# Kernel optimization log

Hardware: AMD Instinct MI355X
Metric: run time of the kernel (lower is better)

Reference implementation:

```python
import jax, jax.numpy as jnp
import numpy as np

N = 131072       # total nodes (B graphs x P nodes)
P = 4096         # nodes per graph
B = 32           # graphs in batch
E = 2097152      # edges (avg degree 16)
IN_DIM = 64
HID = 128
OUT = 16
EPS = 1e-5
SLOPE = 0.01


def _degrees(idx):
    # structural degree, clamped to min 1 (as DGL GraphConv does)
    d = jax.ops.segment_sum(jnp.ones((E,), jnp.float32), idx, num_segments=N)
    return jnp.maximum(d, 1.0)


def _graph_conv(x, W, src, dst, ew):
    # DGL GraphConv, norm='both', bias=False, with scalar edge weights:
    # h = D_out^{-1/2} x ; m_v = sum_{(u->v)} w_e h_u ; out = (D_in^{-1/2} m) W
    h = x * jax.lax.rsqrt(_degrees(src))[:, None]
    m = jax.ops.segment_sum(ew[:, None] * h[src], dst, num_segments=N)  # [N, F]
    return (m * jax.lax.rsqrt(_degrees(dst))[:, None]) @ W


def _graph_norm(x, gamma, beta, alpha):
    # GraphNorm (Cai et al. / PyG, batch=None): stats over all nodes per feature
    mu = jnp.mean(x, axis=0)
    c = x - alpha * mu
    var = jnp.mean(c * c, axis=0)
    return c * jax.lax.rsqrt(var + EPS) * gamma + beta


def _mean_nodes(h, gid):
    # per-graph mean readout; every graph has exactly P nodes
    return jax.ops.segment_sum(h, gid, num_segments=B) / P


def setup_inputs() -> dict:
    key = jax.random.key(0)
    ks = jax.random.split(key, 8)
    src = jax.random.randint(ks[0], (E,), 0, N, dtype=jnp.int32)
    # keep edges within each 4096-node graph block (batched DGL graph)
    dst = (src // P) * P + jax.random.randint(ks[1], (E,), 0, P, dtype=jnp.int32)
    features = jax.random.normal(ks[2], (N, IN_DIM), jnp.float32)
    edge_weights = jax.random.uniform(ks[3], (E,), jnp.float32)
    # kaiming/xavier-scale init approximations
    W1 = jax.random.normal(ks[4], (IN_DIM, HID), jnp.float32) * np.sqrt(2.0 / IN_DIM)
    W2 = jax.random.normal(ks[5], (HID, HID), jnp.float32) * np.sqrt(2.0 / HID)
    Wc = jax.random.normal(ks[6], (OUT, 2 * HID), jnp.float32) * np.sqrt(1.0 / (2 * HID))
    ones = jnp.ones((HID,), jnp.float32)
    zeros = jnp.zeros((HID,), jnp.float32)
    return {
        'features': features, 'edge_weights': edge_weights, 'src': src, 'dst': dst,
        'W1': W1, 'W2': W2, 'Wc': Wc,
        'gamma1': ones, 'beta1': zeros, 'alpha1': ones,
        'gamma2': ones, 'beta2': zeros, 'alpha2': ones,
    }


def reference(features, edge_weights, src, dst, W1, W2, Wc,
              gamma1, beta1, alpha1, gamma2, beta2, alpha2):
    gid = jnp.arange(N, dtype=jnp.int32) // P  # node -> graph id
    h1 = _graph_conv(features, W1, src, dst, edge_weights)
    h1 = jax.nn.leaky_relu(_graph_norm(h1, gamma1, beta1, alpha1), SLOPE)
    r1 = _mean_nodes(h1, gid)                  # [B, HID]
    h2 = _graph_conv(h1, W2, src, dst, edge_weights)
    h2 = jax.nn.leaky_relu(_graph_norm(h2, gamma2, beta2, alpha2), SLOPE)
    r2 = _mean_nodes(h2, gid)                  # [B, HID]
    readouts = jnp.concatenate([r1, r2], axis=1)  # [B, 2*HID]
    return readouts @ Wc.T                     # [B, OUT]
```

## Files before the change

### kernel.cpp

```cpp
#include <hip/hip_runtime.h>
#include <hip/hip_fp16.h>

constexpr int NN   = 131072;
constexpr int PP   = 4096;
constexpr int BG   = 32;
constexpr int EE   = 2097152;
constexpr int IND  = 64;
constexpr int HH   = 128;
constexpr int CAP  = 81920;
constexpr float EPSV   = 1e-5f;
constexpr float SLOPEV = 0.01f;

typedef _Float16 h16x8 __attribute__((ext_vector_type(8)));
typedef float f32x4  __attribute__((ext_vector_type(4)));

__device__ __forceinline__ __half2 bits2h(unsigned u) { __half2 h; *(unsigned*)&h = u; return h; }
__device__ __forceinline__ unsigned h2bits(__half2 h) { return *(unsigned*)&h; }

template <int K>
__device__ __forceinline__ void packw_body(const float* __restrict__ W,
                                           unsigned short* __restrict__ pw, int t) {
    if (t >= K * 16) return;
    int lane = t & 63, nt = (t >> 6) & 7, kt = t >> 9;
    int kbase = kt * 32 + ((lane >> 4) & 3) * 8;
    int col   = nt * 16 + (lane & 15);
    for (int j = 0; j < 8; j++)
        pw[t * 8 + j] = __half_as_ushort(__float2half_rn(W[(kbase + j) * HH + col]));
}

__global__ __launch_bounds__(256) void k_prep(const float* __restrict__ features,
                                              unsigned* __restrict__ f16x,
                                              const float* __restrict__ W1,
                                              unsigned short* __restrict__ pw1,
                                              const float* __restrict__ W2,
                                              unsigned short* __restrict__ pw2,
                                              int* __restrict__ gcur,
                                              float* __restrict__ racc,
                                              unsigned* __restrict__ csr2) {
    int b = blockIdx.x, t = threadIdx.x;
    if (b < 8192) {
        int i = b * 256 + t;
        float4 v = ((const float4*)features)[i];
        __half2 lo = __floats2half2_rn(v.x, v.y);
        __half2 hi = __floats2half2_rn(v.z, v.w);
        ((uint2*)f16x)[i] = make_uint2(h2bits(lo), h2bits(hi));
        return;
    }
    if (b == 8192) {
        if (t < BG) gcur[t * 16] = t * CAP;
        for (int i = t; i < 2 * BG * HH; i += 256) racc[i] = 0.f;
        return;
    }
    if (b < 8197) { packw_body<64>(W1, pw1, (b - 8193) * 256 + t); return; }
    if (b < 8205) { packw_body<128>(W2, pw2, (b - 8197) * 256 + t); return; }
    ((uint4*)csr2)[(b - 8205) * 256 + t] = make_uint4(0, 0, 0, 0);
}

__global__ __launch_bounds__(256) void k_part(const int* __restrict__ src,
                                              const int* __restrict__ dst,
                                              const float* __restrict__ ew,
                                              int* __restrict__ gcur,
                                              uint2* __restrict__ recs) {
    __shared__ int cnt[32];
    __shared__ int start[32];
    __shared__ int gbase[32];
    __shared__ uint2 stage[4096];
    int t = threadIdx.x;
    int ebase = blockIdx.x * 4096;
    if (t < 32) cnt[t] = 0;
    __syncthreads();
    int es[16]; int ed[16]; float ev[16];
#pragma unroll
    for (int k = 0; k < 16; k++) {
        int e = ebase + k * 256 + t;
        es[k] = src[e]; ed[k] = dst[e]; ev[k] = ew[e];
        atomicAdd(&cnt[es[k] >> 12], 1);
    }
    __syncthreads();
    if (t == 0) {
        int run = 0;
        for (int g = 0; g < 32; g++) { start[g] = run; run += cnt[g]; }
    }
    __syncthreads();
    if (t < 32) {
        gbase[t] = atomicAdd(&gcur[t * 16], cnt[t]);
        cnt[t] = start[t];
    }
    __syncthreads();
#pragma unroll
    for (int k = 0; k < 16; k++) {
        int g = es[k] >> 12;
        int pos = atomicAdd(&cnt[g], 1);
        stage[pos] = make_uint2((unsigned)(es[k] & 4095) | ((unsigned)(ed[k] & 4095) << 12) |
                                ((unsigned)g << 24), __float_as_uint(ev[k]));
    }
    __syncthreads();
    for (int i = t; i < 4096; i += 256) {
        uint2 r = stage[i];
        int g = r.x >> 24;
        recs[gbase[g] + (i - start[g])] = r;
    }
}

__global__ __launch_bounds__(1024) void k_hist(const uint2* __restrict__ recs,
                                               const int* __restrict__ gcur,
                                               int* __restrict__ shist,
                                               int* __restrict__ dhist) {
    __shared__ int hs[4096];
    __shared__ int hd[4096];
    int t = threadIdx.x;
    int g = blockIdx.x >> 3, c = blockIdx.x & 7;
    int n = gcur[g * 16] - g * CAP;
    int lo = (n * c) >> 3, hi = (n * (c + 1)) >> 3;
    ((int4*)hs)[t] = make_int4(0, 0, 0, 0);
    ((int4*)hd)[t] = make_int4(0, 0, 0, 0);
    __syncthreads();
    const uint2* base = recs + (size_t)g * CAP;
    for (int i = lo + t; i < hi; i += 1024) {
        unsigned x = base[i].x;
        atomicAdd(&hs[x & 4095], 1);
        atomicAdd(&hd[(x >> 12) & 4095], 1);
    }
    __syncthreads();
    ((int4*)(shist + (size_t)blockIdx.x * 4096))[t] = ((int4*)hs)[t];
    ((int4*)(dhist + (size_t)blockIdx.x * 4096))[t] = ((int4*)hd)[t];
}

__global__ __launch_bounds__(1024) void k_offs(int* __restrict__ shist,
                                               int* __restrict__ dhist,
                                               float* __restrict__ rs_s,
                                               float* __restrict__ rsd,
                                               int* __restrict__ degd,
                                               int* __restrict__ offs) {
    __shared__ int partial[1024];
    int t = threadIdx.x, g = blockIdx.x;
    int sdeg[4] = {0, 0, 0, 0}, ddeg[4] = {0, 0, 0, 0};
#pragma unroll
    for (int c = 0; c < 8; c++) {
        int4 sv = ((const int4*)(shist + (size_t)(g * 8 + c) * 4096))[t];
        int4 dv = ((const int4*)(dhist + (size_t)(g * 8 + c) * 4096))[t];
        sdeg[0] += sv.x; sdeg[1] += sv.y; sdeg[2] += sv.z; sdeg[3] += sv.w;
        ddeg[0] += dv.x; ddeg[1] += dv.y; ddeg[2] += dv.z; ddeg[3] += dv.w;
    }
    int pdeg[4];
#pragma unroll
    for (int j = 0; j < 4; j++) {
        int idx = t * 4 + j;
        int vs = sdeg[j]; if (vs < 1) vs = 1;
        rs_s[g * PP + idx] = rsqrtf((float)vs);
        int vd = ddeg[j]; if (vd < 1) vd = 1;
        rsd[g * PP + idx]  = rsqrtf((float)vd);
        pdeg[j] = (ddeg[j] + 3) & ~3;
        degd[g * PP + idx] = pdeg[j];
    }
    partial[t] = pdeg[0] + pdeg[1] + pdeg[2] + pdeg[3];
    __syncthreads();
    for (int off = 1; off < 1024; off <<= 1) {
        int v = partial[t];
        int add = (t >= off) ? partial[t - off] : 0;
        __syncthreads();
        partial[t] = v + add;
        __syncthreads();
    }
    int run = (t == 0) ? 0 : partial[t - 1];
#pragma unroll
    for (int j = 0; j < 4; j++) {
        int idx = t * 4 + j;
        offs[g * PP + idx] = g * CAP + run;
        int nb = run;
        for (int c = 0; c < 8; c++) {
            size_t hidx = (size_t)(g * 8 + c) * 4096 + idx;
            int v = dhist[hidx];
            dhist[hidx] = nb;
            nb += v;
        }
        run += pdeg[j];
    }
}

__global__ __launch_bounds__(1024) void k_place(const uint2* __restrict__ recs,
                                                const int* __restrict__ gcur,
                                                const int* __restrict__ dhist,
                                                const float* __restrict__ rs_s,
                                                unsigned* __restrict__ csr2) {
    __shared__ int cur[4096];
    __shared__ float rss[4096];
    int t = threadIdx.x;
    int g = blockIdx.x >> 3, c = blockIdx.x & 7;
    int n = gcur[g * 16] - g * CAP;
    int lo = (n * c) >> 3, hi = (n * (c + 1)) >> 3;
    ((int4*)cur)[t] = ((const int4*)(dhist + (size_t)blockIdx.x * 4096))[t];
    ((float4*)rss)[t] = ((const float4*)(rs_s + (size_t)g * PP))[t];
    __syncthreads();
    const uint2* base = recs + (size_t)g * CAP;
    unsigned* cbase = csr2 + (size_t)g * CAP;
    for (int i = lo + t; i < hi; i += 1024) {
        uint2 r = base[i];
        int sl = r.x & 4095, dl = (r.x >> 12) & 4095;
        int pos = atomicAdd(&cur[dl], 1);
        float wf = __uint_as_float(r.y) * rss[sl];
        cbase[pos] = (unsigned)sl | ((unsigned)__half_as_ushort(__float2half(wf)) << 16);
    }
}

__device__ __forceinline__ void edge_acc(unsigned rec, uint2 q, __half2& P01, __half2& P23) {
    unsigned wb = __builtin_amdgcn_perm(rec, rec, 0x03020302u);
    __half2 w2 = bits2h(wb);
    P01 = __hfma2(w2, bits2h(q.x), P01);
    P23 = __hfma2(w2, bits2h(q.y), P23);
}

template <int ROWW>
__device__ __forceinline__ void agg_dual(const uint2* __restrict__ gb, unsigned loff,
                                         const uint4* __restrict__ cs4,
                                         int oa, int ca, int ob, int cb,
                                         __half2& A01, __half2& A23,
                                         __half2& B01, __half2& B23) {
    A01 = __float2half2_rn(0.f); A23 = A01; B01 = A01; B23 = A01;
    unsigned a4 = ((unsigned)oa) >> 2, b4 = ((unsigned)ob) >> 2;
    int c0 = ca < cb ? ca : cb;
    int cm = ca < cb ? cb : ca;
    int nq = c0 >> 2;
    uint4 ra = cs4[a4], rb = cs4[b4];
    for (int k = 0; k < nq; k++) {
        uint2 qa0 = gb[(ra.x & 4095u) * ROWW + loff];
        uint2 qa1 = gb[(ra.y & 4095u) * ROWW + loff];
        uint2 qa2 = gb[(ra.z & 4095u) * ROWW + loff];
        uint2 qa3 = gb[(ra.w & 4095u) * ROWW + loff];
        uint2 qb0 = gb[(rb.x & 4095u) * ROWW + loff];
        uint2 qb1 = gb[(rb.y & 4095u) * ROWW + loff];
        uint2 qb2 = gb[(rb.z & 4095u) * ROWW + loff];
        uint2 qb3 = gb[(rb.w & 4095u) * ROWW + loff];
        uint4 na = cs4[a4 + k + 1];
        uint4 nb = cs4[b4 + k + 1];
        edge_acc(ra.x, qa0, A01, A23); edge_acc(ra.y, qa1, A01, A23);
        edge_acc(ra.z, qa2, A01, A23); edge_acc(ra.w, qa3, A01, A23);
        edge_acc(rb.x, qb0, B01, B23); edge_acc(rb.y, qb1, B01, B23);
        edge_acc(rb.z, qb2, B01, B23); edge_acc(rb.w, qb3, B01, B23);
        ra = na; rb = nb;
    }
    if (cm > c0) {
        bool an = ca > cb;
        unsigned t4 = an ? a4 : b4;
        int kq1 = cm >> 2;
        __half2 E01 = __float2half2_rn(0.f), E23 = E01;
        uint4 rr = cs4[t4 + nq];
        for (int k = nq; k < kq1; k++) {
            uint2 q0 = gb[(rr.x & 4095u) * ROWW + loff];
            uint2 q1 = gb[(rr.y & 4095u) * ROWW + loff];
            uint2 q2 = gb[(rr.z & 4095u) * ROWW + loff];
            uint2 q3 = gb[(rr.w & 4095u) * ROWW + loff];
            uint4 nr = cs4[t4 + k + 1];
            edge_acc(rr.x, q0, E01, E23); edge_acc(rr.y, q1, E01, E23);
            edge_acc(rr.z, q2, E01, E23); edge_acc(rr.w, q3, E01, E23);
            rr = nr;
        }
        if (an) { A01 = __hadd2(A01, E01); A23 = __hadd2(A23, E23); }
        else    { B01 = __hadd2(B01, E01); B23 = __hadd2(B23, E23); }
    }
}

__global__ __launch_bounds__(256) void k_aggemm1(const unsigned* __restrict__ fx,
                                                 const unsigned* __restrict__ csr2,
                                                 const int* __restrict__ offs,
                                                 const int* __restrict__ degd,
                                                 const float* __restrict__ rsd,
                                                 const unsigned short* __restrict__ PW,
                                                 unsigned short* __restrict__ C,
                                                 float* __restrict__ part) {
    constexpr int WP = 36;
    __shared__ __align__(16) unsigned lds[64 * WP];
    __shared__ float s1[HH], s2[HH];
    int t = threadIdx.x;
    if (t < HH) { s1[t] = 0.f; s2[t] = 0.f; }
    int bid = blockIdx.x;
    int xcd = bid & 7, idx = bid >> 3;
    int g = xcd * 4 + (idx >> 6);
    int node0 = g * PP + (idx & 63) * 64;
    int lane = t & 63, wv = t >> 6;
    int q = lane >> 4, ql = lane & 15;
    const uint2* gb = (const uint2*)fx + (size_t)((unsigned)(g * PP)) * 16;
    const uint4* cs4 = (const uint4*)csr2;
    for (int p = 0; p < 2; p++) {
        int lrA = wv * 16 + p * 8 + q * 2;
        int va = node0 + lrA;
        int2 oo = *(const int2*)(offs + va);
        int2 dd = *(const int2*)(degd + va);
        __half2 A01, A23, B01, B23;
        agg_dual<16>(gb, (unsigned)ql, cs4, oo.x, dd.x, oo.y, dd.y, A01, A23, B01, B23);
        float2 rr2 = *(const float2*)(rsd + va);
        __half2 ha = __float2half2_rn(rr2.x), hb = __float2half2_rn(rr2.y);
        __half2 a0 = __hmul2(A01, ha), a1 = __hmul2(A23, ha);
        __half2 b0 = __hmul2(B01, hb), b1 = __hmul2(B23, hb);
        *(uint2*)&lds[lrA * WP + ql * 2]       = make_uint2(h2bits(a0), h2bits(a1));
        *(uint2*)&lds[(lrA + 1) * WP + ql * 2] = make_uint2(h2bits(b0), h2bits(b1));
    }
    __syncthreads();
    int m = lane & 15, quad = lane >> 4;
    h16x8 a[2];
#pragma unroll
    for (int kt = 0; kt < 2; kt++)
        a[kt] = *(const h16x8*)&lds[(wv * 16 + m) * WP + kt * 16 + quad * 4];
#pragma unroll
    for (int nt = 0; nt < 8; nt++) {
        f32x4 acc = {0.f, 0.f, 0.f, 0.f};
#pragma unroll
        for (int kt = 0; kt < 2; kt++) {
            h16x8 b = *(const h16x8*)(PW + ((size_t)(kt * 8 + nt) * 64 + lane) * 8);
            acc = __builtin_amdgcn_mfma_f32_16x16x32_f16(a[kt], b, acc, 0, 0, 0);
        }
        int col = nt * 16 + m;
        int r0 = node0 + wv * 16 + quad * 4;
        float ps = 0.f, pq = 0.f;
#pragma unroll
        for (int r = 0; r < 4; r++) {
            C[(size_t)(r0 + r) * HH + col] = __half_as_ushort(__float2half_rn(acc[r]));
            ps += acc[r]; pq += acc[r] * acc[r];
        }
        atomicAdd(&s1[col], ps);
        atomicAdd(&s2[col], pq);
    }
    __syncthreads();
    if (t < HH) {
        part[bid * 256 + t]      = s1[t];
        part[bid * 256 + HH + t] = s2[t];
    }
}

__global__ __launch_bounds__(256) void k_aggemm2(const unsigned* __restrict__ hsrc,
                                                 const unsigned* __restrict__ csr2,
                                                 const int* __restrict__ offs,
                                                 const int* __restrict__ degd,
                                                 const float* __restrict__ rsd,
                                                 const unsigned short* __restrict__ PW,
                                                 unsigned short* __restrict__ C,
                                                 float* __restrict__ part) {
    constexpr int WP = 68;
    __shared__ __align__(16) unsigned lds[64 * WP];
    __shared__ float s1[HH], s2[HH];
    int t = threadIdx.x;
    if (t < HH) { s1[t] = 0.f; s2[t] = 0.f; }
    int bid = blockIdx.x;
    int xcd = bid & 7, idx = bid >> 3;
    int g = xcd * 4 + (idx >> 6);
    int node0 = g * PP + (idx & 63) * 64;
    int lane = t & 63, wv = t >> 6;
    int half = lane >> 5, sl = lane & 31;
    const uint2* gb = (const uint2*)hsrc + (size_t)((unsigned)(g * PP)) * 32;
    const uint4* cs4 = (const uint4*)csr2;
    for (int p = 0; p < 4; p++) {
        int lrA = wv * 16 + p * 4 + half * 2;
        int va = node0 + lrA;
        int2 oo = *(const int2*)(offs + va);
        int2 dd = *(const int2*)(degd + va);
        __half2 A01, A23, B01, B23;
        agg_dual<32>(gb, (unsigned)sl, cs4, oo.x, dd.x, oo.y, dd.y, A01, A23, B01, B23);
        float2 rr2 = *(const float2*)(rsd + va);
        __half2 ha = __float2half2_rn(rr2.x), hb = __float2half2_rn(rr2.y);
        __half2 a0 = __hmul2(A01, ha), a1 = __hmul2(A23, ha);
        __half2 b0 = __hmul2(B01, hb), b1 = __hmul2(B23, hb);
        *(uint2*)&lds[lrA * WP + sl * 2]       = make_uint2(h2bits(a0), h2bits(a1));
        *(uint2*)&lds[(lrA + 1) * WP + sl * 2] = make_uint2(h2bits(b0), h2bits(b1));
    }
    __syncthreads();
    int m = lane & 15, quad = lane >> 4;
    h16x8 a[4];
#pragma unroll
    for (int kt = 0; kt < 4; kt++)
        a[kt] = *(const h16x8*)&lds[(wv * 16 + m) * WP + kt * 16 + quad * 4];
#pragma unroll
    for (int nt = 0; nt < 8; nt++) {
        f32x4 acc = {0.f, 0.f, 0.f, 0.f};
#pragma unroll
        for (int kt = 0; kt < 4; kt++) {
            h16x8 b = *(const h16x8*)(PW + ((size_t)(kt * 8 + nt) * 64 + lane) * 8);
            acc = __builtin_amdgcn_mfma_f32_16x16x32_f16(a[kt], b, acc, 0, 0, 0);
        }
        int col = nt * 16 + m;
        int r0 = node0 + wv * 16 + quad * 4;
        float ps = 0.f, pq = 0.f;
#pragma unroll
        for (int r = 0; r < 4; r++) {
            C[(size_t)(r0 + r) * HH + col] = __half_as_ushort(__float2half_rn(acc[r]));
            ps += acc[r]; pq += acc[r] * acc[r];
        }
        atomicAdd(&s1[col], ps);
        atomicAdd(&s2[col], pq);
    }
    __syncthreads();
    if (t < HH) {
        part[bid * 256 + t]      = s1[t];
        part[bid * 256 + HH + t] = s2[t];
    }
}

__global__ __launch_bounds__(256) void k_red(const float* __restrict__ part,
                                             float* __restrict__ pb) {
    int t = threadIdx.x, b = blockIdx.x;
    float s = 0.f;
    for (int r = 0; r < 32; r++) s += part[(size_t)(b * 32 + r) * 256 + t];
    pb[b * 256 + t] = s;
}

__global__ void k_coef(const float* __restrict__ pb, const float* __restrict__ gamma,
                       const float* __restrict__ beta, const float* __restrict__ alpha,
                       float* __restrict__ ab) {
    int t = threadIdx.x;
    float s = 0.f;
    for (int b = 0; b < 64; b++) s += pb[b * 256 + t];
    __shared__ float sh[256];
    sh[t] = s;
    __syncthreads();
    if (t < 128) {
        float mu = sh[t] * (1.f / NN);
        float e2 = sh[128 + t] * (1.f / NN);
        float al = alpha[t];
        float var = e2 - (2.f * al - al * al) * mu * mu;
        float a = rsqrtf(var + EPSV) * gamma[t];
        ab[t] = a;
        ab[HH + t] = beta[t] - al * mu * a;
    }
}

template <bool WRITE>
__global__ __launch_bounds__(256) void k_normro(const unsigned* __restrict__ h,
                                                const float* __restrict__ ab,
                                                float* __restrict__ racc,
                                                unsigned* __restrict__ f16o) {
    int fp = threadIdx.x & 63;
    int q  = threadIdx.x >> 6;
    int node0 = blockIdx.x * 64;
    int g = node0 / PP;
    float a0 = ab[2 * fp], a1 = ab[2 * fp + 1];
    float b0 = ab[HH + 2 * fp], b1 = ab[HH + 2 * fp + 1];
    float s0 = 0.f, s1 = 0.f;
    for (int i = q; i < 64; i += 4) {
        size_t idx = (size_t)(node0 + i) * 64 + fp;
        unsigned v = h[idx];
        __half2 hv = bits2h(v);
        float x0 = fmaf(a0, __low2float(hv),  b0); x0 = x0 > 0.f ? x0 : SLOPEV * x0;
        float x1 = fmaf(a1, __high2float(hv), b1); x1 = x1 > 0.f ? x1 : SLOPEV * x1;
        if (WRITE) {
            __half2 o = __floats2half2_rn(x0, x1);
            f16o[idx] = h2bits(o);
        }
        s0 += x0; s1 += x1;
    }
    __shared__ float sh[512];
    sh[threadIdx.x] = s0;
    sh[256 + threadIdx.x] = s1;
    __syncthreads();
    if (q == 0) {
        float t0 = s0 + sh[64 + fp] + sh[128 + fp] + sh[192 + fp];
        float t1 = s1 + sh[256 + 64 + fp] + sh[256 + 128 + fp] + sh[256 + 192 + fp];
        atomicAdd(&racc[g * HH + 2 * fp],     t0);
        atomicAdd(&racc[g * HH + 2 * fp + 1], t1);
    }
}

__global__ void k_final(const float* __restrict__ racc1, const float* __restrict__ racc2,
                        const float* __restrict__ Wc, float* __restrict__ out) {
    int t = threadIdx.x;
    int b = t >> 4, o = t & 15;
    float acc = 0.f;
    for (int f = 0; f < HH; f++) acc += racc1[b * HH + f] * Wc[o * (2 * HH) + f];
    for (int f = 0; f < HH; f++) acc += racc2[b * HH + f] * Wc[o * (2 * HH) + HH + f];
    out[t] = acc * (1.f / PP);
}

extern "C" void kernel_launch(void* const* d_in, const int* in_sizes, int n_in,
                              void* d_out, int out_size, void* d_ws, size_t ws_size,
                              hipStream_t stream) {
    const float* features = (const float*)d_in[0];
    const float* ew       = (const float*)d_in[1];
    const int*   src      = (const int*)d_in[2];
    const int*   dst      = (const int*)d_in[3];
    const float* W1       = (const float*)d_in[4];
    const float* W2       = (const float*)d_in[5];
    const float* Wc       = (const float*)d_in[6];
    const float* gamma1   = (const float*)d_in[7];
    const float* beta1    = (const float*)d_in[8];
    const float* alpha1   = (const float*)d_in[9];
    const float* gamma2   = (const float*)d_in[10];
    const float* beta2    = (const float*)d_in[11];
    const float* alpha2   = (const float*)d_in[12];
    float* out = (float*)d_out;

    char* w = (char*)d_ws;
    int*    gcur   = (int*)(w + 0);
    float*  racc1  = (float*)(w + (16u << 10));
    float*  racc2  = (float*)(w + (32u << 10));
    float*  ab1    = (float*)(w + (48u << 10));
    float*  ab2    = (float*)(w + (52u << 10));
    unsigned short* pw1 = (unsigned short*)(w + (64u << 10));
    unsigned short* pw2 = (unsigned short*)(w + (80u << 10));
    float*  pb     = (float*)(w + (128u << 10));
    float*  rs_s   = (float*)(w + (1024u << 10));
    float*  rsd    = (float*)(w + (1536u << 10));
    int*    degd   = (int*)(w + (2048u << 10));
    int*    offs   = (int*)(w + (2560u << 10));
    float*  part   = (float*)(w + (3u << 20));
    int*    shist  = (int*)(w + (5u << 20));
    int*    dhist  = (int*)(w + (9u << 20));
    unsigned* csr2 = (unsigned*)(w + (13u << 20));
    unsigned* mbuf = (unsigned*)(w + (23u << 20));
    unsigned* hbuf = (unsigned*)(w + (55u << 20));
    uint2*    recs = (uint2*)(w + (87u << 20));
    unsigned* f16x = (unsigned*)(w + (107u << 20));

    k_prep<<<10765, 256, 0, stream>>>(features, f16x, W1, pw1, W2, pw2, gcur, racc1, csr2);

    k_part<<<EE / 4096, 256, 0, stream>>>(src, dst, ew, gcur, recs);
    k_hist<<<BG * 8, 1024, 0, stream>>>(recs, gcur, shist, dhist);
    k_offs<<<BG, 1024, 0, stream>>>(shist, dhist, rs_s, rsd, degd, offs);
    k_place<<<BG * 8, 1024, 0, stream>>>(recs, gcur, dhist, rs_s, csr2);

    k_aggemm1<<<NN / 64, 256, 0, stream>>>(f16x, csr2, offs, degd, rsd,
                                           pw1, (unsigned short*)hbuf, part);
    k_red<<<64, 256, 0, stream>>>(part, pb);
    k_coef<<<1, 256, 0, stream>>>(pb, gamma1, beta1, alpha1, ab1);
    k_normro<true><<<NN / 64, 256, 0, stream>>>(hbuf, ab1, racc1, mbuf);

    k_aggemm2<<<NN / 64, 256, 0, stream>>>(mbuf, csr2, offs, degd, rsd,
                                           pw2, (unsigned short*)hbuf, part);
    k_red<<<64, 256, 0, stream>>>(part, pb);
    k_coef<<<1, 256, 0, stream>>>(pb, gamma2, beta2, alpha2, ab2);
    k_normro<false><<<NN / 64, 256, 0, stream>>>(hbuf, ab2, racc2, nullptr);

    k_final<<<1, 512, 0, stream>>>(racc1, racc2, Wc, out);
}
```

Baseline: 384.1 us.

## Double-buffer CSR gathers in aggregation loop and use nontemporal loads/stores

Restructures the dual-node aggregation loop into a two-stage software pipeline: the feature gathers for the next group of four edges are issued before the current group is accumulated, and CSR records are prefetched two groups ahead. CSR loads, the GEMM output stores, the partial-sum stores and the normalisation pass's loads and stores are marked nontemporal so streaming data is less likely to evict reused feature rows from cache. The deeper pipeline increases register pressure and may lower occupancy. Nontemporal hints on data that a later kernel reads again could also cost cache hits.

```diff
diff --git a/kernel.cpp b/kernel.cpp
--- a/kernel.cpp
+++ b/kernel.cpp
@@ -13,6 +13,7 @@
 
 typedef _Float16 h16x8 __attribute__((ext_vector_type(8)));
 typedef float f32x4  __attribute__((ext_vector_type(4)));
+typedef unsigned u32x4 __attribute__((ext_vector_type(4)));
 
 __device__ __forceinline__ __half2 bits2h(unsigned u) { __half2 h; *(unsigned*)&h = u; return h; }
 __device__ __forceinline__ unsigned h2bits(__half2 h) { return *(unsigned*)&h; }
@@ -211,8 +212,23 @@
 }
 
 template <int ROWW>
+__device__ __forceinline__ void gath(const uint2* __restrict__ gb, unsigned loff, u32x4 r,
+                                     uint2& d0, uint2& d1, uint2& d2, uint2& d3) {
+    d0 = gb[(r[0] & 4095u) * ROWW + loff];
+    d1 = gb[(r[1] & 4095u) * ROWW + loff];
+    d2 = gb[(r[2] & 4095u) * ROWW + loff];
+    d3 = gb[(r[3] & 4095u) * ROWW + loff];
+}
+
+__device__ __forceinline__ void macc(u32x4 r, uint2 q0, uint2 q1, uint2 q2, uint2 q3,
+                                     __half2& P01, __half2& P23) {
+    edge_acc(r[0], q0, P01, P23); edge_acc(r[1], q1, P01, P23);
+    edge_acc(r[2], q2, P01, P23); edge_acc(r[3], q3, P01, P23);
+}
+
+template <int ROWW>
 __device__ __forceinline__ void agg_dual(const uint2* __restrict__ gb, unsigned loff,
-                                         const uint4* __restrict__ cs4,
+                                         const u32x4* __restrict__ cs4,
                                          int oa, int ca, int ob, int cb,
                                          __half2& A01, __half2& A23,
                                          __half2& B01, __half2& B23) {
@@ -221,38 +237,48 @@
     int c0 = ca < cb ? ca : cb;
     int cm = ca < cb ? cb : ca;
     int nq = c0 >> 2;
-    uint4 ra = cs4[a4], rb = cs4[b4];
-    for (int k = 0; k < nq; k++) {
-        uint2 qa0 = gb[(ra.x & 4095u) * ROWW + loff];
-        uint2 qa1 = gb[(ra.y & 4095u) * ROWW + loff];
-        uint2 qa2 = gb[(ra.z & 4095u) * ROWW + loff];
-        uint2 qa3 = gb[(ra.w & 4095u) * ROWW + loff];
-        uint2 qb0 = gb[(rb.x & 4095u) * ROWW + loff];
-        uint2 qb1 = gb[(rb.y & 4095u) * ROWW + loff];
-        uint2 qb2 = gb[(rb.z & 4095u) * ROWW + loff];
-        uint2 qb3 = gb[(rb.w & 4095u) * ROWW + loff];
-        uint4 na = cs4[a4 + k + 1];
-        uint4 nb = cs4[b4 + k + 1];
-        edge_acc(ra.x, qa0, A01, A23); edge_acc(ra.y, qa1, A01, A23);
-        edge_acc(ra.z, qa2, A01, A23); edge_acc(ra.w, qa3, A01, A23);
-        edge_acc(rb.x, qb0, B01, B23); edge_acc(rb.y, qb1, B01, B23);
-        edge_acc(rb.z, qb2, B01, B23); edge_acc(rb.w, qb3, B01, B23);
-        ra = na; rb = nb;
+    if (nq > 0) {
+        u32x4 ra0 = __builtin_nontemporal_load(cs4 + a4);
+        u32x4 rb0 = __builtin_nontemporal_load(cs4 + b4);
+        u32x4 ra1 = __builtin_nontemporal_load(cs4 + a4 + 1);
+        u32x4 rb1 = __builtin_nontemporal_load(cs4 + b4 + 1);
+        uint2 A0, A1, A2, A3, B0, B1, B2, B3;
+        uint2 C0, C1, C2, C3, D0, D1, D2, D3;
+        gath<ROWW>(gb, loff, ra0, A0, A1, A2, A3);
+        gath<ROWW>(gb, loff, rb0, B0, B1, B2, B3);
+        int k = 0;
+        for (; k + 2 <= nq; k += 2) {
+            gath<ROWW>(gb, loff, ra1, C0, C1, C2, C3);
+            gath<ROWW>(gb, loff, rb1, D0, D1, D2, D3);
+            u32x4 ra2 = __builtin_nontemporal_load(cs4 + a4 + k + 2);
+            u32x4 rb2 = __builtin_nontemporal_load(cs4 + b4 + k + 2);
+            macc(ra0, A0, A1, A2, A3, A01, A23);
+            macc(rb0, B0, B1, B2, B3, B01, B23);
+            gath<ROWW>(gb, loff, ra2, A0, A1, A2, A3);
+            gath<ROWW>(gb, loff, rb2, B0, B1, B2, B3);
+            u32x4 ra3 = __builtin_nontemporal_load(cs4 + a4 + k + 3);
+            u32x4 rb3 = __builtin_nontemporal_load(cs4 + b4 + k + 3);
+            macc(ra1, C0, C1, C2, C3, A01, A23);
+            macc(rb1, D0, D1, D2, D3, B01, B23);
+            ra0 = ra2; rb0 = rb2; ra1 = ra3; rb1 = rb3;
+        }
+        if (k < nq) {
+            macc(ra0, A0, A1, A2, A3, A01, A23);
+            macc(rb0, B0, B1, B2, B3, B01, B23);
+        }
     }
     if (cm > c0) {
         bool an = ca > cb;
         unsigned t4 = an ? a4 : b4;
         int kq1 = cm >> 2;
         __half2 E01 = __float2half2_rn(0.f), E23 = E01;
-        uint4 rr = cs4[t4 + nq];
-        for (int k = nq; k < kq1; k++) {
-            uint2 q0 = gb[(rr.x & 4095u) * ROWW + loff];
-            uint2 q1 = gb[(rr.y & 4095u) * ROWW + loff];
-            uint2 q2 = gb[(rr.z & 4095u) * ROWW + loff];
-            uint2 q3 = gb[(rr.w & 4095u) * ROWW + loff];
-            uint4 nr = cs4[t4 + k + 1];
-            edge_acc(rr.x, q0, E01, E23); edge_acc(rr.y, q1, E01, E23);
-            edge_acc(rr.z, q2, E01, E23); edge_acc(rr.w, q3, E01, E23);
+        int nq0 = c0 >> 2;
+        u32x4 rr = __builtin_nontemporal_load(cs4 + t4 + nq0);
+        for (int k = nq0; k < kq1; k++) {
+            uint2 q0, q1, q2, q3;
+            gath<ROWW>(gb, loff, rr, q0, q1, q2, q3);
+            u32x4 nr = __builtin_nontemporal_load(cs4 + t4 + k + 1);
+            macc(rr, q0, q1, q2, q3, E01, E23);
             rr = nr;
         }
         if (an) { A01 = __hadd2(A01, E01); A23 = __hadd2(A23, E23); }
@@ -280,7 +306,8 @@
     int lane = t & 63, wv = t >> 6;
     int q = lane >> 4, ql = lane & 15;
     const uint2* gb = (const uint2*)fx + (size_t)((unsigned)(g * PP)) * 16;
-    const uint4* cs4 = (const uint4*)csr2;
+    const u32x4* cs4 = (const u32x4*)csr2;
+#pragma unroll
     for (int p = 0; p < 2; p++) {
         int lrA = wv * 16 + p * 8 + q * 2;
         int va = node0 + lrA;
@@ -314,7 +341,9 @@
         float ps = 0.f, pq = 0.f;
 #pragma unroll
         for (int r = 0; r < 4; r++) {
-            C[(size_t)(r0 + r) * HH + col] = __half_as_ushort(__float2half_rn(acc[r]));
+            __builtin_nontemporal_store(
+                (unsigned short)__half_as_ushort(__float2half_rn(acc[r])),
+                &C[(size_t)(r0 + r) * HH + col]);
             ps += acc[r]; pq += acc[r] * acc[r];
         }
         atomicAdd(&s1[col], ps);
@@ -322,8 +351,8 @@
     }
     __syncthreads();
     if (t < HH) {
-        part[bid * 256 + t]      = s1[t];
-        part[bid * 256 + HH + t] = s2[t];
+        __builtin_nontemporal_store(s1[t], &part[bid * 256 + t]);
+        __builtin_nontemporal_store(s2[t], &part[bid * 256 + HH + t]);
     }
 }
 
@@ -347,7 +376,8 @@
     int lane = t & 63, wv = t >> 6;
     int half = lane >> 5, sl = lane & 31;
     const uint2* gb = (const uint2*)hsrc + (size_t)((unsigned)(g * PP)) * 32;
-    const uint4* cs4 = (const uint4*)csr2;
+    const u32x4* cs4 = (const u32x4*)csr2;
+#pragma unroll
     for (int p = 0; p < 4; p++) {
         int lrA = wv * 16 + p * 4 + half * 2;
         int va = node0 + lrA;
@@ -381,7 +411,9 @@
         float ps = 0.f, pq = 0.f;
 #pragma unroll
         for (int r = 0; r < 4; r++) {
-            C[(size_t)(r0 + r) * HH + col] = __half_as_ushort(__float2half_rn(acc[r]));
+            __builtin_nontemporal_store(
+                (unsigned short)__half_as_ushort(__float2half_rn(acc[r])),
+                &C[(size_t)(r0 + r) * HH + col]);
             ps += acc[r]; pq += acc[r] * acc[r];
         }
         atomicAdd(&s1[col], ps);
@@ -389,8 +421,8 @@
     }
     __syncthreads();
     if (t < HH) {
-        part[bid * 256 + t]      = s1[t];
-        part[bid * 256 + HH + t] = s2[t];
+        __builtin_nontemporal_store(s1[t], &part[bid * 256 + t]);
+        __builtin_nontemporal_store(s2[t], &part[bid * 256 + HH + t]);
     }
 }
 
@@ -436,13 +468,13 @@
     float s0 = 0.f, s1 = 0.f;
     for (int i = q; i < 64; i += 4) {
         size_t idx = (size_t)(node0 + i) * 64 + fp;
-        unsigned v = h[idx];
+        unsigned v = __builtin_nontemporal_load(&h[idx]);
         __half2 hv = bits2h(v);
         float x0 = fmaf(a0, __low2float(hv),  b0); x0 = x0 > 0.f ? x0 : SLOPEV * x0;
         float x1 = fmaf(a1, __high2float(hv), b1); x1 = x1 > 0.f ? x1 : SLOPEV * x1;
         if (WRITE) {
             __half2 o = __floats2half2_rn(x0, x1);
-            f16o[idx] = h2bits(o);
+            __builtin_nontemporal_store(h2bits(o), &f16o[idx]);
         }
         s0 += x0; s1 += x1;
     }
```

New measurement: 419.4 us. 9.2% more time.
